# Optimization experiments

Measured on AMD Instinct MI355X. Metric: run time of the kernel, lower is better.

Reference implementation:

```python
import jax, jax.numpy as jnp
import numpy as np

B, H, W, C = 8, 64, 64, 64


def setup_inputs() -> dict:
    key = jax.random.key(0)
    ks = jax.random.split(key, 9)
    s = 1.0 / np.sqrt(C)
    return {
        "x": jax.random.normal(ks[0], (B, H, W, C), dtype=jnp.float32),
        "wq": jax.random.uniform(ks[1], (C, C), jnp.float32, -s, s),
        "bq": jax.random.uniform(ks[2], (C,), jnp.float32, -s, s),
        "wk": jax.random.uniform(ks[3], (C, C), jnp.float32, -s, s),
        "bk": jax.random.uniform(ks[4], (C,), jnp.float32, -s, s),
        "wv": jax.random.uniform(ks[5], (C, C), jnp.float32, -s, s),
        "bv": jax.random.uniform(ks[6], (C,), jnp.float32, -s, s),
        "wp": jax.random.uniform(ks[7], (C, C), jnp.float32, -s, s),
        "bp": jax.random.uniform(ks[8], (C,), jnp.float32, -s, s),
    }


def reference(x, wq, bq, wk, bk, wv, bv, wp, bp):
    b, h, w, c = x.shape
    n = h * w
    xf = x.reshape(b, n, c)
    scale = c ** (-0.5)
    q = xf @ wq.T + bq  # [B,N,C]
    k = xf @ wk.T + bk
    v = xf @ wv.T + bv
    center_idx = (h // 2) * w + (w // 2)
    central = q[:, center_idx, :][:, None, :]           # [B,1,C]
    qb = jnp.broadcast_to(central, (b, n, c))           # rank-1 broadcast query
    pos = jnp.arange(n)
    dist = jnp.sqrt(((pos // w - h // 2) ** 2 + (pos % w - w // 2) ** 2).astype(jnp.float32))
    weights = jnp.exp(1.0 - dist)                       # [N]
    qw = qb * weights[None, :, None]
    attn = jnp.einsum('bnc,bmc->bnm', qw, k) * scale    # dense [B,N,N] (memory-bound)
    attn = jax.nn.softmax(attn, axis=-1)
    out = jnp.einsum('bnm,bmc->bnc', attn, v)
    out = out @ wp.T + bp
    return out.reshape(b, h, w, c)
```

## Files before the change

### kernel.cpp

```cpp
#include <hip/hip_runtime.h>

#define BB 8
#define NN 4096
#define CC 64
#define CENTER (32*64 + 32)
#define GTILE 16
#define MS 32
#define MSL (NN/MS)
#define CUT 64

struct Geom {
    short gid[2049];
    short g2d2[64];
    int ng;
};

constexpr Geom makeGeom() {
    Geom t{};
    bool occ[2049] = {};
    for (int y = 0; y < 64; ++y)
        for (int x = 0; x < 64; ++x) {
            int dy = y - 32, dx = x - 32;
            occ[dy*dy + dx*dx] = true;
        }
    int g = 0;
    for (int i = 0; i < CUT; ++i) {
        if (occ[i]) { t.gid[i] = (short)g; t.g2d2[g] = (short)i; ++g; }
        else t.gid[i] = (short)-1;
    }
    t.ng = g;
    for (int i = CUT; i <= 2048; ++i) t.gid[i] = occ[i] ? (short)g : (short)-1;
    return t;
}

constexpr int NGN = makeGeom().ng;
constexpr int NT  = (NGN + 1 + GTILE - 1) / GTILE;
constexpr int GE  = NT * GTILE;
static_assert(NGN + 1 <= GE, "group padding");
static_assert(GE == 32, "k_red decode assumes GE=32");
static_assert(MS * 8 == 256, "blockIdx decode shift");
__constant__ Geom GEOM = makeGeom();

constexpr int CST_WVPT = 0;
constexpr int CST_BVP  = 4096;
constexpr int CST_U    = 4160;
constexpr int CST_T    = 4672;
constexpr int CST_SIZE = 4736;

constexpr int OFF_CST  = 0;
constexpr int OFF_S    = CST_SIZE;
constexpr int OFF_VP   = OFF_S + BB*NN;
constexpr int OFF_PART = OFF_VP + BB*NN*CC;
constexpr int OFF_ZP   = OFF_PART + BB*MS*GE*CC;
constexpr int OFF_OG   = OFF_ZP + BB*MS*GE;

__global__ __launch_bounds__(256) void k_prep(
    const float* __restrict__ x,
    const float* __restrict__ wq, const float* __restrict__ bq,
    const float* __restrict__ wk, const float* __restrict__ bk,
    const float* __restrict__ wv, const float* __restrict__ bv,
    const float* __restrict__ wp,
    float* __restrict__ cst)
{
    const int tid = threadIdx.x;
    const int blk = blockIdx.x;
    if (blk < 8) {
        __shared__ float q_s[CC];
        const int b = blk;
        if (tid < CC) {
            const float* xc = x + ((size_t)b*NN + CENTER)*CC;
            float a = bq[tid];
            for (int i = 0; i < CC; ++i) a += xc[i] * wq[tid*CC + i];
            q_s[tid] = a;
        }
        __syncthreads();
        if (tid < CC) {
            float a = 0.f;
            for (int c = 0; c < CC; ++c) a += q_s[c] * wk[c*CC + tid];
            cst[CST_U + b*CC + tid] = a;
        }
        if (tid == 64) {
            float a = 0.f;
            for (int c = 0; c < CC; ++c) a += q_s[c] * bk[c];
            cst[CST_T + b] = a;
        }
    } else if (blk < 24) {
        const int idx = (blk - 8)*256 + tid;
        const int i = idx >> 6, c = idx & 63;
        float a = 0.f;
        for (int j = 0; j < CC; ++j) a += wp[c*CC + j] * wv[j*CC + i];
        cst[CST_WVPT + idx] = a;
    } else {
        if (tid < CC) {
            float a = 0.f;
            for (int j = 0; j < CC; ++j) a += wp[tid*CC + j] * bv[j];
            cst[CST_BVP + tid] = a;
        }
    }
}

__global__ __launch_bounds__(256) void k_vps(
    const float* __restrict__ x, const float* __restrict__ cst,
    float* __restrict__ s_out, float* __restrict__ vp_out)
{
    const int tid = threadIdx.x;
    const int cq  = blockIdx.x & 3;
    const int row = (blockIdx.x >> 2)*256 + tid;
    const int b   = blockIdx.x >> 6;

    float4 xr[16];
    const float4* x4 = (const float4*)(x + (size_t)row * CC);
    #pragma unroll
    for (int i = 0; i < 16; ++i) xr[i] = x4[i];

    if (cq == 0) {
        const float* u = cst + CST_U + b*CC;
        float sa = cst[CST_T + b];
        #pragma unroll
        for (int i4 = 0; i4 < 16; ++i4) {
            sa += xr[i4].x*u[i4*4+0] + xr[i4].y*u[i4*4+1]
                + xr[i4].z*u[i4*4+2] + xr[i4].w*u[i4*4+3];
        }
        s_out[row] = sa * 0.125f;
    }

    const int c0 = cq * 16;
    float4 acc[4];
    #pragma unroll
    for (int k = 0; k < 4; ++k) {
        acc[k].x = cst[CST_BVP + c0 + k*4 + 0];
        acc[k].y = cst[CST_BVP + c0 + k*4 + 1];
        acc[k].z = cst[CST_BVP + c0 + k*4 + 2];
        acc[k].w = cst[CST_BVP + c0 + k*4 + 3];
    }
    #pragma unroll
    for (int i = 0; i < 64; ++i) {
        const float xv = ((const float*)xr)[i];
        const float* wr = cst + CST_WVPT + i*CC + c0;
        #pragma unroll
        for (int k = 0; k < 4; ++k) {
            acc[k].x += xv * wr[k*4+0];
            acc[k].y += xv * wr[k*4+1];
            acc[k].z += xv * wr[k*4+2];
            acc[k].w += xv * wr[k*4+3];
        }
    }
    float4* vp4 = (float4*)vp_out + (size_t)row*16 + cq*4;
    #pragma unroll
    for (int k = 0; k < 4; ++k) vp4[k] = acc[k];
}

#define FMA4(A, E, V) do { (A).x += (E)*(V).x; (A).y += (E)*(V).y; \
                           (A).z += (E)*(V).z; (A).w += (E)*(V).w; } while(0)

__global__ __launch_bounds__(256) void k_attn(
    const float* __restrict__ sA, const float* __restrict__ vpA,
    float* __restrict__ part, float* __restrict__ zpart)
{
    __shared__ __align__(16) float Es[MSL*GTILE];
    __shared__ __align__(16) float red[4*GTILE*GTILE*4];
    __shared__ float zred[4*GTILE];
    __shared__ float w_s[GTILE];

    const int tid = threadIdx.x;
    const int b   = blockIdx.x & 7;
    const int ms  = (blockIdx.x >> 3) & (MS - 1);
    const int gt  = blockIdx.x >> 8;
    const int g0  = gt * GTILE;
    const int m0  = ms * MSL;

    if (tid < GTILE) {
        const int g = g0 + tid;
        w_s[tid] = (g < NGN) ? __expf(1.f - sqrtf((float)GEOM.g2d2[g])) : 0.f;
    }
    __syncthreads();

    const int gE = tid & 15;
    const int mE = tid >> 4;
    const float wg = w_s[gE];
    const int c4 = tid & 15;

    float zacc = 0.f;
    float4 acc[GTILE];
    #pragma unroll
    for (int g = 0; g < GTILE; ++g) acc[g] = make_float4(0.f, 0.f, 0.f, 0.f);

    const float* s_row = sA + b*NN + m0;
    const float4* vp4  = (const float4*)vpA + ((size_t)b*NN + m0)*16;
    const float4* E4   = (const float4*)Es;

    #pragma unroll
    for (int p = 0; p < MSL/16; ++p) {
        const int ml = mE + 16*p;
        const float e = __expf(wg * s_row[ml]);
        Es[ml*GTILE + gE] = e;
        zacc += e;
    }
    __syncthreads();
    #pragma unroll
    for (int p = 0; p < MSL/16; ++p) {
        const int ml = mE + 16*p;
        const float4 v4 = vp4[(size_t)ml*16 + c4];
        float4 e4;
        e4 = E4[ml*4 + 0];
        FMA4(acc[0],  e4.x, v4); FMA4(acc[1],  e4.y, v4);
        FMA4(acc[2],  e4.z, v4); FMA4(acc[3],  e4.w, v4);
        e4 = E4[ml*4 + 1];
        FMA4(acc[4],  e4.x, v4); FMA4(acc[5],  e4.y, v4);
        FMA4(acc[6],  e4.z, v4); FMA4(acc[7],  e4.w, v4);
        e4 = E4[ml*4 + 2];
        FMA4(acc[8],  e4.x, v4); FMA4(acc[9],  e4.y, v4);
        FMA4(acc[10], e4.z, v4); FMA4(acc[11], e4.w, v4);
        e4 = E4[ml*4 + 3];
        FMA4(acc[12], e4.x, v4); FMA4(acc[13], e4.y, v4);
        FMA4(acc[14], e4.z, v4); FMA4(acc[15], e4.w, v4);
    }
    __syncthreads();

    const int l  = tid & 63;
    const int wv = tid >> 6;
    #pragma unroll
    for (int g = 0; g < GTILE; ++g) {
        acc[g].x += __shfl_xor(acc[g].x, 16, 64);
        acc[g].y += __shfl_xor(acc[g].y, 16, 64);
        acc[g].z += __shfl_xor(acc[g].z, 16, 64);
        acc[g].w += __shfl_xor(acc[g].w, 16, 64);
        acc[g].x += __shfl_xor(acc[g].x, 32, 64);
        acc[g].y += __shfl_xor(acc[g].y, 32, 64);
        acc[g].z += __shfl_xor(acc[g].z, 32, 64);
        acc[g].w += __shfl_xor(acc[g].w, 32, 64);
    }
    zacc += __shfl_xor(zacc, 16, 64);
    zacc += __shfl_xor(zacc, 32, 64);

    float4* red4 = (float4*)red;
    if (l < 16) {
        #pragma unroll
        for (int g = 0; g < GTILE; ++g)
            red4[(wv*GTILE + g)*GTILE + l] = acc[g];
        zred[wv*16 + l] = zacc;
    }
    __syncthreads();

    {
        const int g = tid >> 4, c = tid & 15;
        float4 o0 = red4[(0*GTILE + g)*GTILE + c];
        float4 o1 = red4[(1*GTILE + g)*GTILE + c];
        float4 o2 = red4[(2*GTILE + g)*GTILE + c];
        float4 o3 = red4[(3*GTILE + g)*GTILE + c];
        o0.x += o1.x + o2.x + o3.x;
        o0.y += o1.y + o2.y + o3.y;
        o0.z += o1.z + o2.z + o3.z;
        o0.w += o1.w + o2.w + o3.w;
        ((float4*)part)[(size_t)((b*MS + ms)*GE + g0 + g)*16 + c] = o0;
        if (tid < 16) {
            float Zg = zred[tid] + zred[16+tid] + zred[32+tid] + zred[48+tid];
            zpart[(b*MS + ms)*GE + g0 + tid] = Zg;
        }
    }
}

__global__ __launch_bounds__(256) void k_red(
    const float* __restrict__ part, const float* __restrict__ zpart,
    const float* __restrict__ bp, float* __restrict__ og)
{
    __shared__ float ared[4*CC];
    __shared__ float zr[4];

    const int tid = threadIdx.x;
    const int bg  = blockIdx.x;
    const int b   = bg >> 5, g = bg & 31;
    const int q   = tid >> 6;
    const int c   = tid & 63;

    float a = 0.f, z = 0.f;
    #pragma unroll
    for (int j = 0; j < MS/4; ++j) {
        const int ms = q*(MS/4) + j;
        a += part[(size_t)((b*MS + ms)*GE + g)*CC + c];
        z += zpart[(b*MS + ms)*GE + g];
    }
    ared[q*CC + c] = a;
    if (c == 0) zr[q] = z;
    __syncthreads();
    if (tid < CC) {
        const float at = ared[tid] + ared[CC + tid] + ared[2*CC + tid] + ared[3*CC + tid];
        const float zt = zr[0] + zr[1] + zr[2] + zr[3];
        og[(size_t)bg*CC + tid] = at / zt + bp[tid];
    }
}

__global__ __launch_bounds__(256) void k_out(
    const float* __restrict__ og, float* __restrict__ out)
{
    const int i4 = blockIdx.x * 256 + threadIdx.x;
    const int c4 = i4 & 15;
    const int n  = (i4 >> 4) & (NN - 1);
    const int b  = i4 >> 16;
    const int dy = (n >> 6) - 32, dx = (n & 63) - 32;
    const int g  = GEOM.gid[dy*dy + dx*dx];
    ((float4*)out)[i4] = ((const float4*)og)[(size_t)(b*GE + g)*16 + c4];
}

extern "C" void kernel_launch(void* const* d_in, const int* in_sizes, int n_in,
                              void* d_out, int out_size, void* d_ws, size_t ws_size,
                              hipStream_t stream) {
    const float* x  = (const float*)d_in[0];
    const float* wq = (const float*)d_in[1];
    const float* bq = (const float*)d_in[2];
    const float* wk = (const float*)d_in[3];
    const float* bk = (const float*)d_in[4];
    const float* wv = (const float*)d_in[5];
    const float* bv = (const float*)d_in[6];
    const float* wp = (const float*)d_in[7];
    const float* bp = (const float*)d_in[8];
    float* ws = (float*)d_ws;

    k_prep<<<25, 256, 0, stream>>>(x, wq, bq, wk, bk, wv, bv, wp, ws + OFF_CST);
    k_vps<<<512, 256, 0, stream>>>(x, ws + OFF_CST, ws + OFF_S, ws + OFF_VP);
    k_attn<<<NT*MS*8, 256, 0, stream>>>(ws + OFF_S, ws + OFF_VP,
                                        ws + OFF_PART, ws + OFF_ZP);
    k_red<<<BB*GE, 256, 0, stream>>>(ws + OFF_PART, ws + OFF_ZP,
                                     bp, ws + OFF_OG);
    k_out<<<2048, 256, 0, stream>>>(ws + OFF_OG, (float*)d_out);
}
```

Before: 104.3 us.

## Aggregate softmax-weighted x per group and apply value/output projections once per group

Uses linearity of the value and output projections: the attention-weighted sum is taken over raw x rows instead of projected v, and Wv and Wp are applied once per (batch, distance group) in the final kernel. This removes the full B×N×C value-projection pass and its global intermediate buffer. It also fuses the query/key prep and score computation into the main kernel, which stages x tiles in padded shared memory, cutting five launches to three. The cost is recomputing the central query per block and a serial per-block tail of small matvecs.

```diff
diff --git a/kernel.cpp b/kernel.cpp
--- a/kernel.cpp
+++ b/kernel.cpp
@@ -4,9 +4,10 @@
 #define NN 4096
 #define CC 64
 #define CENTER (32*64 + 32)
-#define GTILE 16
-#define MS 32
-#define MSL (NN/MS)
+#define MS 64
+#define RR (NN/MS)
+#define GE 32
+#define XPAD 68
 #define CUT 64
 
 struct Geom {
@@ -34,259 +35,176 @@
 }
 
 constexpr int NGN = makeGeom().ng;
-constexpr int NT  = (NGN + 1 + GTILE - 1) / GTILE;
-constexpr int GE  = NT * GTILE;
 static_assert(NGN + 1 <= GE, "group padding");
-static_assert(GE == 32, "k_red decode assumes GE=32");
-static_assert(MS * 8 == 256, "blockIdx decode shift");
+static_assert(GE == 32, "decode assumes GE=32");
+static_assert(MS * RR == NN, "geometry");
 __constant__ Geom GEOM = makeGeom();
 
-constexpr int CST_WVPT = 0;
-constexpr int CST_BVP  = 4096;
-constexpr int CST_U    = 4160;
-constexpr int CST_T    = 4672;
-constexpr int CST_SIZE = 4736;
-
-constexpr int OFF_CST  = 0;
-constexpr int OFF_S    = CST_SIZE;
-constexpr int OFF_VP   = OFF_S + BB*NN;
-constexpr int OFF_PART = OFF_VP + BB*NN*CC;
+constexpr int OFF_PART = 0;
 constexpr int OFF_ZP   = OFF_PART + BB*MS*GE*CC;
 constexpr int OFF_OG   = OFF_ZP + BB*MS*GE;
 
-__global__ __launch_bounds__(256) void k_prep(
+#define FMA4(A, E, V) do { (A).x += (E)*(V).x; (A).y += (E)*(V).y; \
+                           (A).z += (E)*(V).z; (A).w += (E)*(V).w; } while(0)
+
+__global__ __launch_bounds__(256) void k_main(
     const float* __restrict__ x,
     const float* __restrict__ wq, const float* __restrict__ bq,
     const float* __restrict__ wk, const float* __restrict__ bk,
-    const float* __restrict__ wv, const float* __restrict__ bv,
-    const float* __restrict__ wp,
-    float* __restrict__ cst)
+    float* __restrict__ part, float* __restrict__ zpart)
 {
+    __shared__ __align__(16) float xs[RR*XPAD];
+    __shared__ float qs[CC];
+    __shared__ float us[CC];
+    __shared__ __align__(16) float ss[RR];
+    __shared__ float ts_s;
+
     const int tid = threadIdx.x;
-    const int blk = blockIdx.x;
-    if (blk < 8) {
-        __shared__ float q_s[CC];
-        const int b = blk;
-        if (tid < CC) {
-            const float* xc = x + ((size_t)b*NN + CENTER)*CC;
-            float a = bq[tid];
-            for (int i = 0; i < CC; ++i) a += xc[i] * wq[tid*CC + i];
-            q_s[tid] = a;
-        }
-        __syncthreads();
-        if (tid < CC) {
-            float a = 0.f;
-            for (int c = 0; c < CC; ++c) a += q_s[c] * wk[c*CC + tid];
-            cst[CST_U + b*CC + tid] = a;
-        }
-        if (tid == 64) {
-            float a = 0.f;
-            for (int c = 0; c < CC; ++c) a += q_s[c] * bk[c];
-            cst[CST_T + b] = a;
-        }
-    } else if (blk < 24) {
-        const int idx = (blk - 8)*256 + tid;
-        const int i = idx >> 6, c = idx & 63;
-        float a = 0.f;
-        for (int j = 0; j < CC; ++j) a += wp[c*CC + j] * wv[j*CC + i];
-        cst[CST_WVPT + idx] = a;
-    } else {
-        if (tid < CC) {
-            float a = 0.f;
-            for (int j = 0; j < CC; ++j) a += wp[tid*CC + j] * bv[j];
-            cst[CST_BVP + tid] = a;
-        }
-    }
-}
-
-__global__ __launch_bounds__(256) void k_vps(
-    const float* __restrict__ x, const float* __restrict__ cst,
-    float* __restrict__ s_out, float* __restrict__ vp_out)
-{
-    const int tid = threadIdx.x;
-    const int cq  = blockIdx.x & 3;
-    const int row = (blockIdx.x >> 2)*256 + tid;
-    const int b   = blockIdx.x >> 6;
-
-    float4 xr[16];
-    const float4* x4 = (const float4*)(x + (size_t)row * CC);
+    const int b   = blockIdx.x & 7;
+    const int ms  = blockIdx.x >> 3;
+    const int m0  = ms * RR;
+
+    float4 xr[4];
+    const float4* x4 = (const float4*)x + ((size_t)b*NN + m0)*16;
     #pragma unroll
-    for (int i = 0; i < 16; ++i) xr[i] = x4[i];
-
-    if (cq == 0) {
-        const float* u = cst + CST_U + b*CC;
-        float sa = cst[CST_T + b];
-        #pragma unroll
-        for (int i4 = 0; i4 < 16; ++i4) {
-            sa += xr[i4].x*u[i4*4+0] + xr[i4].y*u[i4*4+1]
-                + xr[i4].z*u[i4*4+2] + xr[i4].w*u[i4*4+3];
-        }
-        s_out[row] = sa * 0.125f;
-    }
-
-    const int c0 = cq * 16;
-    float4 acc[4];
+    for (int k = 0; k < 4; ++k) xr[k] = x4[tid + 256*k];
+
+    if (tid < CC) {
+        const float* xc = x + ((size_t)b*NN + CENTER)*CC;
+        const float* wr = wq + tid*CC;
+        float a0 = bq[tid], a1 = 0.f, a2 = 0.f, a3 = 0.f;
+        #pragma unroll
+        for (int i = 0; i < CC; i += 4) {
+            a0 += xc[i+0]*wr[i+0]; a1 += xc[i+1]*wr[i+1];
+            a2 += xc[i+2]*wr[i+2]; a3 += xc[i+3]*wr[i+3];
+        }
+        qs[tid] = a0+a1+a2+a3;
+    }
     #pragma unroll
     for (int k = 0; k < 4; ++k) {
-        acc[k].x = cst[CST_BVP + c0 + k*4 + 0];
-        acc[k].y = cst[CST_BVP + c0 + k*4 + 1];
-        acc[k].z = cst[CST_BVP + c0 + k*4 + 2];
-        acc[k].w = cst[CST_BVP + c0 + k*4 + 3];
-    }
-    #pragma unroll
-    for (int i = 0; i < 64; ++i) {
-        const float xv = ((const float*)xr)[i];
-        const float* wr = cst + CST_WVPT + i*CC + c0;
-        #pragma unroll
-        for (int k = 0; k < 4; ++k) {
-            acc[k].x += xv * wr[k*4+0];
-            acc[k].y += xv * wr[k*4+1];
-            acc[k].z += xv * wr[k*4+2];
-            acc[k].w += xv * wr[k*4+3];
-        }
-    }
-    float4* vp4 = (float4*)vp_out + (size_t)row*16 + cq*4;
-    #pragma unroll
-    for (int k = 0; k < 4; ++k) vp4[k] = acc[k];
-}
-
-#define FMA4(A, E, V) do { (A).x += (E)*(V).x; (A).y += (E)*(V).y; \
-                           (A).z += (E)*(V).z; (A).w += (E)*(V).w; } while(0)
-
-__global__ __launch_bounds__(256) void k_attn(
-    const float* __restrict__ sA, const float* __restrict__ vpA,
-    float* __restrict__ part, float* __restrict__ zpart)
+        const int idx = tid + 256*k;
+        *(float4*)&xs[(idx >> 4)*XPAD + (idx & 15)*4] = xr[k];
+    }
+    __syncthreads();
+
+    if (tid < CC) {
+        float a0=0.f,a1=0.f,a2=0.f,a3=0.f;
+        #pragma unroll
+        for (int j = 0; j < CC; j += 4) {
+            a0 += qs[j+0]*wk[(j+0)*CC + tid];
+            a1 += qs[j+1]*wk[(j+1)*CC + tid];
+            a2 += qs[j+2]*wk[(j+2)*CC + tid];
+            a3 += qs[j+3]*wk[(j+3)*CC + tid];
+        }
+        us[tid] = a0+a1+a2+a3;
+    } else if (tid == CC) {
+        float a = 0.f;
+        for (int j = 0; j < CC; ++j) a += qs[j]*bk[j];
+        ts_s = a;
+    }
+    __syncthreads();
+
+    if (tid < 2*RR) {
+        const int r = tid >> 1, h = tid & 1;
+        const float* xrow = &xs[r*XPAD + h*32];
+        const float* uh = &us[h*32];
+        float a0=0.f,a1=0.f,a2=0.f,a3=0.f;
+        #pragma unroll
+        for (int i = 0; i < 32; i += 4) {
+            a0 += xrow[i+0]*uh[i+0]; a1 += xrow[i+1]*uh[i+1];
+            a2 += xrow[i+2]*uh[i+2]; a3 += xrow[i+3]*uh[i+3];
+        }
+        float p = a0+a1+a2+a3;
+        p += __shfl_xor(p, 1, 64);
+        if (h == 0) ss[r] = (p + ts_s) * 0.125f;
+    }
+    __syncthreads();
+
+    const int g  = tid >> 3;
+    const int i0 = (tid & 7) * 8;
+    const float wg = (g < NGN) ? __expf(1.f - sqrtf((float)GEOM.g2d2[g])) : 0.f;
+    float4 y0 = make_float4(0.f,0.f,0.f,0.f), y1 = make_float4(0.f,0.f,0.f,0.f);
+    float z = 0.f;
+    #pragma unroll 4
+    for (int r4 = 0; r4 < RR; r4 += 4) {
+        const float4 s4 = *(const float4*)&ss[r4];
+        float e;
+        e = __expf(wg*s4.x); z += e;
+        FMA4(y0, e, *(const float4*)&xs[(r4+0)*XPAD + i0]);
+        FMA4(y1, e, *(const float4*)&xs[(r4+0)*XPAD + i0 + 4]);
+        e = __expf(wg*s4.y); z += e;
+        FMA4(y0, e, *(const float4*)&xs[(r4+1)*XPAD + i0]);
+        FMA4(y1, e, *(const float4*)&xs[(r4+1)*XPAD + i0 + 4]);
+        e = __expf(wg*s4.z); z += e;
+        FMA4(y0, e, *(const float4*)&xs[(r4+2)*XPAD + i0]);
+        FMA4(y1, e, *(const float4*)&xs[(r4+2)*XPAD + i0 + 4]);
+        e = __expf(wg*s4.w); z += e;
+        FMA4(y0, e, *(const float4*)&xs[(r4+3)*XPAD + i0]);
+        FMA4(y1, e, *(const float4*)&xs[(r4+3)*XPAD + i0 + 4]);
+    }
+    float4* p4 = (float4*)part + ((size_t)((b*MS + ms)*GE + g)*CC + i0)/4;
+    p4[0] = y0; p4[1] = y1;
+    if ((tid & 7) == 0) zpart[(b*MS + ms)*GE + g] = z;
+}
+
+__global__ __launch_bounds__(256) void k_final(
+    const float* __restrict__ part, const float* __restrict__ zpart,
+    const float* __restrict__ wv, const float* __restrict__ bv,
+    const float* __restrict__ wp, const float* __restrict__ bp,
+    float* __restrict__ og)
 {
-    __shared__ __align__(16) float Es[MSL*GTILE];
-    __shared__ __align__(16) float red[4*GTILE*GTILE*4];
-    __shared__ float zred[4*GTILE];
-    __shared__ float w_s[GTILE];
+    __shared__ float yred[4*CC];
+    __shared__ float ysh[CC];
+    __shared__ float hsh[CC];
+    __shared__ float zsh;
 
     const int tid = threadIdx.x;
-    const int b   = blockIdx.x & 7;
-    const int ms  = (blockIdx.x >> 3) & (MS - 1);
-    const int gt  = blockIdx.x >> 8;
-    const int g0  = gt * GTILE;
-    const int m0  = ms * MSL;
-
-    if (tid < GTILE) {
-        const int g = g0 + tid;
-        w_s[tid] = (g < NGN) ? __expf(1.f - sqrtf((float)GEOM.g2d2[g])) : 0.f;
-    }
-    __syncthreads();
-
-    const int gE = tid & 15;
-    const int mE = tid >> 4;
-    const float wg = w_s[gE];
-    const int c4 = tid & 15;
-
-    float zacc = 0.f;
-    float4 acc[GTILE];
-    #pragma unroll
-    for (int g = 0; g < GTILE; ++g) acc[g] = make_float4(0.f, 0.f, 0.f, 0.f);
-
-    const float* s_row = sA + b*NN + m0;
-    const float4* vp4  = (const float4*)vpA + ((size_t)b*NN + m0)*16;
-    const float4* E4   = (const float4*)Es;
-
-    #pragma unroll
-    for (int p = 0; p < MSL/16; ++p) {
-        const int ml = mE + 16*p;
-        const float e = __expf(wg * s_row[ml]);
-        Es[ml*GTILE + gE] = e;
-        zacc += e;
-    }
-    __syncthreads();
-    #pragma unroll
-    for (int p = 0; p < MSL/16; ++p) {
-        const int ml = mE + 16*p;
-        const float4 v4 = vp4[(size_t)ml*16 + c4];
-        float4 e4;
-        e4 = E4[ml*4 + 0];
-        FMA4(acc[0],  e4.x, v4); FMA4(acc[1],  e4.y, v4);
-        FMA4(acc[2],  e4.z, v4); FMA4(acc[3],  e4.w, v4);
-        e4 = E4[ml*4 + 1];
-        FMA4(acc[4],  e4.x, v4); FMA4(acc[5],  e4.y, v4);
-        FMA4(acc[6],  e4.z, v4); FMA4(acc[7],  e4.w, v4);
-        e4 = E4[ml*4 + 2];
-        FMA4(acc[8],  e4.x, v4); FMA4(acc[9],  e4.y, v4);
-        FMA4(acc[10], e4.z, v4); FMA4(acc[11], e4.w, v4);
-        e4 = E4[ml*4 + 3];
-        FMA4(acc[12], e4.x, v4); FMA4(acc[13], e4.y, v4);
-        FMA4(acc[14], e4.z, v4); FMA4(acc[15], e4.w, v4);
-    }
-    __syncthreads();
-
-    const int l  = tid & 63;
-    const int wv = tid >> 6;
-    #pragma unroll
-    for (int g = 0; g < GTILE; ++g) {
-        acc[g].x += __shfl_xor(acc[g].x, 16, 64);
-        acc[g].y += __shfl_xor(acc[g].y, 16, 64);
-        acc[g].z += __shfl_xor(acc[g].z, 16, 64);
-        acc[g].w += __shfl_xor(acc[g].w, 16, 64);
-        acc[g].x += __shfl_xor(acc[g].x, 32, 64);
-        acc[g].y += __shfl_xor(acc[g].y, 32, 64);
-        acc[g].z += __shfl_xor(acc[g].z, 32, 64);
-        acc[g].w += __shfl_xor(acc[g].w, 32, 64);
-    }
-    zacc += __shfl_xor(zacc, 16, 64);
-    zacc += __shfl_xor(zacc, 32, 64);
-
-    float4* red4 = (float4*)red;
-    if (l < 16) {
-        #pragma unroll
-        for (int g = 0; g < GTILE; ++g)
-            red4[(wv*GTILE + g)*GTILE + l] = acc[g];
-        zred[wv*16 + l] = zacc;
-    }
-    __syncthreads();
-
-    {
-        const int g = tid >> 4, c = tid & 15;
-        float4 o0 = red4[(0*GTILE + g)*GTILE + c];
-        float4 o1 = red4[(1*GTILE + g)*GTILE + c];
-        float4 o2 = red4[(2*GTILE + g)*GTILE + c];
-        float4 o3 = red4[(3*GTILE + g)*GTILE + c];
-        o0.x += o1.x + o2.x + o3.x;
-        o0.y += o1.y + o2.y + o3.y;
-        o0.z += o1.z + o2.z + o3.z;
-        o0.w += o1.w + o2.w + o3.w;
-        ((float4*)part)[(size_t)((b*MS + ms)*GE + g0 + g)*16 + c] = o0;
-        if (tid < 16) {
-            float Zg = zred[tid] + zred[16+tid] + zred[32+tid] + zred[48+tid];
-            zpart[(b*MS + ms)*GE + g0 + tid] = Zg;
-        }
-    }
-}
-
-__global__ __launch_bounds__(256) void k_red(
-    const float* __restrict__ part, const float* __restrict__ zpart,
-    const float* __restrict__ bp, float* __restrict__ og)
-{
-    __shared__ float ared[4*CC];
-    __shared__ float zr[4];
-
-    const int tid = threadIdx.x;
-    const int bg  = blockIdx.x;
-    const int b   = bg >> 5, g = bg & 31;
-    const int q   = tid >> 6;
-    const int c   = tid & 63;
-
-    float a = 0.f, z = 0.f;
+    const int b = blockIdx.x >> 5, g = blockIdx.x & 31;
+    const int i = tid & 63, q = tid >> 6;
+
+    float a = 0.f;
     #pragma unroll
     for (int j = 0; j < MS/4; ++j) {
         const int ms = q*(MS/4) + j;
-        a += part[(size_t)((b*MS + ms)*GE + g)*CC + c];
-        z += zpart[(b*MS + ms)*GE + g];
-    }
-    ared[q*CC + c] = a;
-    if (c == 0) zr[q] = z;
-    __syncthreads();
-    if (tid < CC) {
-        const float at = ared[tid] + ared[CC + tid] + ared[2*CC + tid] + ared[3*CC + tid];
-        const float zt = zr[0] + zr[1] + zr[2] + zr[3];
-        og[(size_t)bg*CC + tid] = at / zt + bp[tid];
+        a += part[((size_t)(b*MS + ms)*GE + g)*CC + i];
+    }
+    yred[q*CC + i] = a;
+
+    float zv = 0.f;
+    if (tid < 64) {
+        zv = zpart[(b*MS + tid)*GE + g];
+        zv += __shfl_xor(zv, 1, 64);
+        zv += __shfl_xor(zv, 2, 64);
+        zv += __shfl_xor(zv, 4, 64);
+        zv += __shfl_xor(zv, 8, 64);
+        zv += __shfl_xor(zv, 16, 64);
+        zv += __shfl_xor(zv, 32, 64);
+        if (tid == 0) zsh = zv;
+    }
+    __syncthreads();
+    if (tid < CC)
+        ysh[tid] = yred[tid] + yred[CC+tid] + yred[2*CC+tid] + yred[3*CC+tid];
+    __syncthreads();
+    if (tid < CC) {
+        const float* wr = wv + tid*CC;
+        float a0=0.f,a1=0.f,a2=0.f,a3=0.f;
+        #pragma unroll
+        for (int j = 0; j < CC; j += 4) {
+            a0 += wr[j+0]*ysh[j+0]; a1 += wr[j+1]*ysh[j+1];
+            a2 += wr[j+2]*ysh[j+2]; a3 += wr[j+3]*ysh[j+3];
+        }
+        hsh[tid] = (a0+a1+a2+a3)/zsh + bv[tid];
+    }
+    __syncthreads();
+    if (tid < CC) {
+        const float* wr = wp + tid*CC;
+        float a0=bp[tid],a1=0.f,a2=0.f,a3=0.f;
+        #pragma unroll
+        for (int j = 0; j < CC; j += 4) {
+            a0 += wr[j+0]*hsh[j+0]; a1 += wr[j+1]*hsh[j+1];
+            a2 += wr[j+2]*hsh[j+2]; a3 += wr[j+3]*hsh[j+3];
+        }
+        og[((size_t)b*GE + g)*CC + tid] = a0+a1+a2+a3;
     }
 }
 
@@ -296,10 +214,10 @@
     const int i4 = blockIdx.x * 256 + threadIdx.x;
     const int c4 = i4 & 15;
     const int n  = (i4 >> 4) & (NN - 1);
-    const int b  = i4 >> 16;
+    const int bb = i4 >> 16;
     const int dy = (n >> 6) - 32, dx = (n & 63) - 32;
     const int g  = GEOM.gid[dy*dy + dx*dx];
-    ((float4*)out)[i4] = ((const float4*)og)[(size_t)(b*GE + g)*16 + c4];
+    ((float4*)out)[i4] = ((const float4*)og)[(size_t)(bb*GE + g)*16 + c4];
 }
 
 extern "C" void kernel_launch(void* const* d_in, const int* in_sizes, int n_in,
@@ -316,11 +234,9 @@
     const float* bp = (const float*)d_in[8];
     float* ws = (float*)d_ws;
 
-    k_prep<<<25, 256, 0, stream>>>(x, wq, bq, wk, bk, wv, bv, wp, ws + OFF_CST);
-    k_vps<<<512, 256, 0, stream>>>(x, ws + OFF_CST, ws + OFF_S, ws + OFF_VP);
-    k_attn<<<NT*MS*8, 256, 0, stream>>>(ws + OFF_S, ws + OFF_VP,
-                                        ws + OFF_PART, ws + OFF_ZP);
-    k_red<<<BB*GE, 256, 0, stream>>>(ws + OFF_PART, ws + OFF_ZP,
-                                     bp, ws + OFF_OG);
+    k_main<<<MS*8, 256, 0, stream>>>(x, wq, bq, wk, bk,
+                                     ws + OFF_PART, ws + OFF_ZP);
+    k_final<<<BB*GE, 256, 0, stream>>>(ws + OFF_PART, ws + OFF_ZP,
+                                       wv, bv, wp, bp, ws + OFF_OG);
     k_out<<<2048, 256, 0, stream>>>(ws + OFF_OG, (float*)d_out);
 }
```

New measurement: 89.21 us. 1.17x faster.
